# Performance work log

Hardware: AMD Instinct MI355X
Metric: run time of the kernel (lower is better)

## Reference

```python
import jax, jax.numpy as jnp
import numpy as np

DIM = 1024
NUM_HEADS = 16
HEAD_DIM = DIM // NUM_HEADS
SCALE = HEAD_DIM ** -0.5


def setup_inputs() -> dict:
    key = jax.random.key(0)
    ks = jax.random.split(key, 7)
    b, n = 2, 2048
    x = jax.random.normal(ks[0], (b, n, DIM), dtype=jnp.float32)
    s = DIM ** -0.5
    Wq = jax.random.normal(ks[1], (DIM, DIM), dtype=jnp.float32) * s
    bq = jax.random.normal(ks[2], (DIM,), dtype=jnp.float32) * 0.01
    Wk = jax.random.normal(ks[3], (DIM, DIM), dtype=jnp.float32) * s
    bk = jax.random.normal(ks[4], (DIM,), dtype=jnp.float32) * 0.01
    Wv = jax.random.normal(ks[5], (DIM, DIM), dtype=jnp.float32) * s
    bv = jax.random.normal(ks[6], (DIM,), dtype=jnp.float32) * 0.01
    return {"x": x, "Wq": Wq, "bq": bq, "Wk": Wk, "bk": bk, "Wv": Wv, "bv": bv}


def reference(x, Wq, bq, Wk, bk, Wv, bv):
    b, n, _ = x.shape
    # Linear projections (torch Linear: x @ W.T + b; here W stored as [in, out])
    q = x @ Wq + bq
    k = x @ Wk + bk
    v = x @ Wv + bv
    # split heads: [b, n, h*d] -> [b, h, n, d]
    split = lambda t: t.reshape(b, n, NUM_HEADS, HEAD_DIM).transpose(0, 2, 1, 3)
    q, k, v = split(q), split(k), split(v)
    sim = jnp.einsum('bhid,bhjd->bhij', q, k) * SCALE
    attn = jax.nn.softmax(sim, axis=-1)
    out = jnp.einsum('bhij,bhjd->bhid', attn, v)
    return out.transpose(0, 2, 1, 3).reshape(b, n, DIM)
```

## Files before the change

### kernel.cpp

```cpp
#include <hip/hip_runtime.h>
#include <cstdint>
#include <cstddef>

#define NB    2
#define SEQ   2048
#define DIMC  1024
#define NH    16
#define HDIM  64
#define MROWS (NB*SEQ)
#define NFEAT (3*DIMC)
#define KVBLK 64
#define NT    (SEQ/KVBLK)

typedef _Float16 half8 __attribute__((ext_vector_type(8)));
typedef _Float16 half4 __attribute__((ext_vector_type(4)));
typedef _Float16 half2v __attribute__((ext_vector_type(2)));
typedef __fp16   fp16x2 __attribute__((ext_vector_type(2)));
typedef float    f32x4 __attribute__((ext_vector_type(4)));

typedef const __attribute__((address_space(1))) void* gas_ptr;
typedef __attribute__((address_space(3))) void*       las_ptr;

__device__ __forceinline__ void gload_lds16(const void* g, void* l) {
    __builtin_amdgcn_global_load_lds((gas_ptr)g, (las_ptr)l, 16, 0, 0);
}

__device__ __forceinline__ int swz4(int r) { return (r ^ (r >> 2)) & 3; }

__device__ __forceinline__ float fast_exp2(float x) {
    float r;
    asm("v_exp_f32 %0, %1" : "=v"(r) : "v"(x));
    return r;
}

__device__ __forceinline__ half2v pk_f16(float a, float b) {
    fp16x2 r = __builtin_amdgcn_cvt_pkrtz(a, b);
    return __builtin_bit_cast(half2v, r);
}

__global__ __launch_bounds__(256) void k_convert_x(const float* __restrict__ x,
                                                   _Float16* __restrict__ x16) {
    int i = (blockIdx.x * 256 + threadIdx.x) * 4;
    float4 v = *reinterpret_cast<const float4*>(x + i);
    half4 h = { (_Float16)v.x, (_Float16)v.y, (_Float16)v.z, (_Float16)v.w };
    *reinterpret_cast<half4*>(x16 + i) = h;
}

__global__ __launch_bounds__(256) void k_transpose_w(const float* __restrict__ Wq,
                                                     const float* __restrict__ Wk,
                                                     const float* __restrict__ Wv,
                                                     _Float16* __restrict__ wt) {
    __shared__ float tile[64][65];
    const int bid  = blockIdx.x;
    const int midx = bid >> 8;
    const int t2   = bid & 255;
    const int i0   = (t2 >> 4) * 64;
    const int o0   = (t2 & 15) * 64;
    const float* W = (midx == 0) ? Wq : (midx == 1 ? Wk : Wv);
    const int tid  = threadIdx.x;
    #pragma unroll
    for (int p = 0; p < 4; ++p) {
        int id = p * 256 + tid;
        int r = id >> 4, c4 = (id & 15) * 4;
        float4 v = *reinterpret_cast<const float4*>(W + (size_t)(i0 + r) * DIMC + o0 + c4);
        tile[r][c4 + 0] = v.x; tile[r][c4 + 1] = v.y;
        tile[r][c4 + 2] = v.z; tile[r][c4 + 3] = v.w;
    }
    __syncthreads();
    #pragma unroll
    for (int p = 0; p < 4; ++p) {
        int id = p * 256 + tid;
        int oc = id >> 4, i4 = (id & 15) * 4;
        half4 h = { (_Float16)tile[i4 + 0][oc], (_Float16)tile[i4 + 1][oc],
                    (_Float16)tile[i4 + 2][oc], (_Float16)tile[i4 + 3][oc] };
        *reinterpret_cast<half4*>(wt + (size_t)(midx * DIMC + o0 + oc) * DIMC + i0 + i4) = h;
    }
}

__global__ __launch_bounds__(256) void k_qkv_gemm(
    const _Float16* __restrict__ x16, const _Float16* __restrict__ wt,
    const float* __restrict__ bq, const float* __restrict__ bk, const float* __restrict__ bv,
    _Float16* __restrict__ q16, _Float16* __restrict__ k16, _Float16* __restrict__ vt16)
{
    __shared__ __align__(16) char sraw[49152];
    const int tid = threadIdx.x;
    const int lane = tid & 63;
    const int w = tid >> 6, wm = w >> 1, wn = w & 1;
    const int lr = lane & 15, lg = lane >> 4;
    const int bn = blockIdx.x % (NFEAT / 128);
    const int bm = blockIdx.x / (NFEAT / 128);
    const int m0 = bm * 128, n0 = bn * 128;

    const f32x4 zero4 = {0.f, 0.f, 0.f, 0.f};
    f32x4 acc[4][4];
    #pragma unroll
    for (int i = 0; i < 4; ++i)
        #pragma unroll
        for (int j = 0; j < 4; ++j) acc[i][j] = zero4;

    auto stage = [&](int buf, int kt) {
        const int k0 = kt * 32;
        char* Adst = sraw + buf * 8192;
        char* Bdst = sraw + 24576 + buf * 8192;
        #pragma unroll
        for (int t = 0; t < 2; ++t) {
            int slot = t * 256 + tid;
            int row = slot >> 2, ch = slot & 3;
            int chg = ch ^ swz4(row);
            gload_lds16(x16 + (size_t)(m0 + row) * DIMC + k0 + chg * 8, Adst + slot * 16);
            gload_lds16(wt  + (size_t)(n0 + row) * DIMC + k0 + chg * 8, Bdst + slot * 16);
        }
    };

    stage(0, 0);
    stage(1, 1);
    for (int kt = 0; kt < DIMC / 32; ++kt) {
        if (kt < DIMC / 32 - 1) asm volatile("s_waitcnt vmcnt(4)" ::: "memory");
        else                    asm volatile("s_waitcnt vmcnt(0)" ::: "memory");
        __builtin_amdgcn_s_barrier();
        if (kt + 2 < DIMC / 32) stage((kt + 2) % 3, kt + 2);
        const char* Ab = sraw + (kt % 3) * 8192;
        const char* Bb = sraw + 24576 + (kt % 3) * 8192;
        half8 af[4], bf[4];
        #pragma unroll
        for (int mb = 0; mb < 4; ++mb) {
            int row = wm * 64 + mb * 16 + lr;
            af[mb] = *(const half8*)(Ab + row * 64 + ((lg ^ swz4(row)) << 4));
        }
        #pragma unroll
        for (int nb = 0; nb < 4; ++nb) {
            int col = wn * 64 + nb * 16 + lr;
            bf[nb] = *(const half8*)(Bb + col * 64 + ((lg ^ swz4(col)) << 4));
        }
        #pragma unroll
        for (int mb = 0; mb < 4; ++mb)
            #pragma unroll
            for (int nb = 0; nb < 4; ++nb)
                acc[mb][nb] = __builtin_amdgcn_mfma_f32_16x16x32_f16(af[mb], bf[nb], acc[mb][nb], 0, 0, 0);
    }

    const int sec = n0 >> 10;
    const float* bias = (sec == 0) ? bq : (sec == 1 ? bk : bv);
    const float scl = (sec == 0) ? 0.125f * 1.44269504088896f : 1.0f;
    float bfv[4];
    #pragma unroll
    for (int nb = 0; nb < 4; ++nb)
        bfv[nb] = bias[(n0 & 1023) + wn * 64 + nb * 16 + lr];

    if (sec < 2) {
        _Float16* dst = (sec == 0) ? q16 : k16;
        #pragma unroll
        for (int mb = 0; mb < 4; ++mb)
            #pragma unroll
            for (int i2 = 0; i2 < 4; ++i2) {
                int rg = m0 + wm * 64 + mb * 16 + lg * 4 + i2;
                int bb = rg >> 11, nn = rg & (SEQ - 1);
                #pragma unroll
                for (int nb = 0; nb < 4; ++nb) {
                    int f1 = (n0 & 1023) + wn * 64 + nb * 16 + lr;
                    int hh = f1 >> 6, dd = f1 & 63;
                    dst[((size_t)(bb * NH + hh) * SEQ + nn) * HDIM + dd] =
                        (_Float16)((acc[mb][nb][i2] + bfv[nb]) * scl);
                }
            }
    } else {
        __syncthreads();
        char* lt = sraw;
        #pragma unroll
        for (int mb = 0; mb < 4; ++mb)
            #pragma unroll
            for (int nb = 0; nb < 4; ++nb) {
                int c  = wn * 64 + nb * 16 + lr;
                int r0 = wm * 64 + mb * 16 + lg * 4;
                half4 hv = { (_Float16)(acc[mb][nb][0] + bfv[nb]),
                             (_Float16)(acc[mb][nb][1] + bfv[nb]),
                             (_Float16)(acc[mb][nb][2] + bfv[nb]),
                             (_Float16)(acc[mb][nb][3] + bfv[nb]) };
                *(half4*)(lt + c * 272 + r0 * 2) = hv;
            }
        __syncthreads();
        #pragma unroll
        for (int p = 0; p < 8; ++p) {
            int id = p * 256 + tid;
            int c = id >> 4, r8 = (id & 15) * 8;
            half8 hv = *(const half8*)(lt + c * 272 + r8 * 2);
            int f1 = (n0 & 1023) + c;
            int hh = f1 >> 6, dd = f1 & 63;
            int rg = m0 + r8;
            int bb = rg >> 11, nn = rg & (SEQ - 1);
            *(half8*)(vt16 + ((size_t)(bb * NH + hh) * HDIM + dd) * SEQ + nn) = hv;
        }
    }
}

__global__ __launch_bounds__(512, 4) void k_attn(
    const _Float16* __restrict__ q16, const _Float16* __restrict__ k16,
    const _Float16* __restrict__ vt16, float* __restrict__ out)
{
    __shared__ __align__(16) char lds[65536];
    const int tid = threadIdx.x, lane = tid & 63, w = tid >> 6;
    const int lr = lane & 15, lg = lane >> 4;
    const int sub = w >> 2;
    const int qg  = w & 3;
    const int swz = (blockIdx.x & 7) * 64 + (blockIdx.x >> 3);
    const int bh = swz >> 4;
    const int qt = swz & 15;
    const int qrow0 = qt * 128 + qg * 32;
    const _Float16* qh = q16 + (size_t)bh * SEQ * HDIM;
    const _Float16* kh = k16 + (size_t)bh * SEQ * HDIM;
    const _Float16* vh = vt16 + (size_t)bh * HDIM * SEQ;

    const int srow = tid >> 3;
    const int scg  = (tid & 7) ^ (srow & 7);

    auto stageKV = [&](int buf, int t) {
        const int jA = t * KVBLK, jB = (16 + t) * KVBLK;
        gload_lds16(kh + (size_t)(jA + srow) * HDIM + scg * 8,
                    lds + buf * 8192 + tid * 16);
        gload_lds16(kh + (size_t)(jB + srow) * HDIM + scg * 8,
                    lds + 16384 + buf * 8192 + tid * 16);
        gload_lds16(vh + (size_t)srow * SEQ + jA + scg * 8,
                    lds + 32768 + buf * 8192 + tid * 16);
        gload_lds16(vh + (size_t)srow * SEQ + jB + scg * 8,
                    lds + 49152 + buf * 8192 + tid * 16);
    };

    half8 aq[2][2];
    #pragma unroll
    for (int g = 0; g < 2; ++g)
        #pragma unroll
        for (int kc = 0; kc < 2; ++kc)
            aq[g][kc] = *(const half8*)(qh + (size_t)(qrow0 + g * 16 + lr) * HDIM + kc * 32 + lg * 8);

    const f32x4 zero4 = {0.f, 0.f, 0.f, 0.f};
    f32x4 l4[2] = { zero4, zero4 };
    f32x4 oacc[2][4];
    #pragma unroll
    for (int g = 0; g < 2; ++g)
        #pragma unroll
        for (int i = 0; i < 4; ++i) oacc[g][i] = zero4;

    stageKV(0, 0);
    for (int t = 0; t < 16; ++t) {
        __syncthreads();
        if (t + 1 < 16) stageKV((t + 1) & 1, t + 1);
        const char* Kb = lds + sub * 16384 + (t & 1) * 8192;
        const char* Vb = lds + 32768 + sub * 16384 + (t & 1) * 8192;

        f32x4 s0[4], s1[4];
        __builtin_amdgcn_s_setprio(1);
        #pragma unroll
        for (int jb = 0; jb < 4; ++jb) {
            int row = jb * 16 + lr;
            half8 k0 = *(const half8*)(Kb + row * 128 + (((0 + lg) ^ (row & 7)) << 4));
            half8 k1 = *(const half8*)(Kb + row * 128 + (((4 + lg) ^ (row & 7)) << 4));
            f32x4 a0 = __builtin_amdgcn_mfma_f32_16x16x32_f16(k0, aq[0][0], zero4, 0, 0, 0);
            f32x4 a1 = __builtin_amdgcn_mfma_f32_16x16x32_f16(k0, aq[1][0], zero4, 0, 0, 0);
            a0 = __builtin_amdgcn_mfma_f32_16x16x32_f16(k1, aq[0][1], a0, 0, 0, 0);
            a1 = __builtin_amdgcn_mfma_f32_16x16x32_f16(k1, aq[1][1], a1, 0, 0, 0);
            s0[jb] = a0; s1[jb] = a1;
        }
        __builtin_amdgcn_s_setprio(0);

        half4 pf0[4], pf1[4];
        #pragma unroll
        for (int jb = 0; jb < 4; ++jb) {
            #pragma unroll
            for (int i = 0; i < 4; ++i) s0[jb][i] = fast_exp2(s0[jb][i]);
            l4[0] += s0[jb];
            half2v w0 = pk_f16(s0[jb][0], s0[jb][1]);
            half2v w1 = pk_f16(s0[jb][2], s0[jb][3]);
            pf0[jb] = half4{ w0.x, w0.y, w1.x, w1.y };
        }
        #pragma unroll
        for (int jb = 0; jb < 4; ++jb) {
            #pragma unroll
            for (int i = 0; i < 4; ++i) s1[jb][i] = fast_exp2(s1[jb][i]);
            l4[1] += s1[jb];
            half2v w0 = pk_f16(s1[jb][0], s1[jb][1]);
            half2v w1 = pk_f16(s1[jb][2], s1[jb][3]);
            pf1[jb] = half4{ w0.x, w0.y, w1.x, w1.y };
        }

        __builtin_amdgcn_s_setprio(1);
        #pragma unroll
        for (int db = 0; db < 4; ++db) {
            int row = db * 16 + lr;
            const char* vrow = Vb + row * 128;
            #pragma unroll
            for (int jb = 0; jb < 4; ++jb) {
                half4 vf = *(const half4*)(vrow + (((jb * 2 + (lg >> 1)) ^ (row & 7)) << 4)
                                           + ((lg & 1) << 3));
                oacc[0][db] = __builtin_amdgcn_mfma_f32_16x16x16f16(pf0[jb], vf, oacc[0][db], 0, 0, 0);
                oacc[1][db] = __builtin_amdgcn_mfma_f32_16x16x16f16(pf1[jb], vf, oacc[1][db], 0, 0, 0);
            }
        }
        __builtin_amdgcn_s_setprio(0);
    }

    __syncthreads();
    char* xch = lds;
    if (sub == 1) {
        char* sl = xch + (qg * 2) * 5120;
        #pragma unroll
        for (int g = 0; g < 2; ++g) {
            #pragma unroll
            for (int db = 0; db < 4; ++db)
                *(f32x4*)(sl + g * 5120 + db * 1024 + lane * 16) = oacc[g][db];
            *(f32x4*)(sl + g * 5120 + 4096 + lane * 16) = l4[g];
        }
    }
    __syncthreads();
    if (sub == 0) {
        char* sl = xch + (qg * 2) * 5120;
        #pragma unroll
        for (int g = 0; g < 2; ++g) {
            #pragma unroll
            for (int db = 0; db < 4; ++db)
                oacc[g][db] += *(const f32x4*)(sl + g * 5120 + db * 1024 + lane * 16);
            l4[g] += *(const f32x4*)(sl + g * 5120 + 4096 + lane * 16);
        }
        const int bb = bh >> 4, hh = bh & 15;
        #pragma unroll
        for (int g = 0; g < 2; ++g) {
            float l_i = (l4[g][0] + l4[g][1]) + (l4[g][2] + l4[g][3]);
            l_i += __shfl_xor(l_i, 16);
            l_i += __shfl_xor(l_i, 32);
            float rlq[4];
            #pragma unroll
            for (int i = 0; i < 4; ++i)
                rlq[i] = 1.0f / __shfl(l_i, lg * 4 + i);
            #pragma unroll
            for (int db = 0; db < 4; ++db)
                #pragma unroll
                for (int i = 0; i < 4; ++i) {
                    int nn = qrow0 + g * 16 + lg * 4 + i;
                    out[((size_t)bb * SEQ + nn) * DIMC + hh * HDIM + db * 16 + lr] =
                        oacc[g][db][i] * rlq[i];
                }
        }
    }
}

extern "C" void kernel_launch(void* const* d_in, const int* in_sizes, int n_in,
                              void* d_out, int out_size, void* d_ws, size_t ws_size,
                              hipStream_t stream)
{
    const float* x  = (const float*)d_in[0];
    const float* Wq = (const float*)d_in[1];
    const float* bq = (const float*)d_in[2];
    const float* Wk = (const float*)d_in[3];
    const float* bk = (const float*)d_in[4];
    const float* Wv = (const float*)d_in[5];
    const float* bv = (const float*)d_in[6];
    float* out = (float*)d_out;

    char* ws = (char*)d_ws;
    _Float16* x16  = (_Float16*)ws;
    _Float16* wt   = (_Float16*)(ws + ((size_t)8  << 20));
    _Float16* q16  = (_Float16*)(ws + ((size_t)14 << 20));
    _Float16* k16  = (_Float16*)(ws + ((size_t)22 << 20));
    _Float16* vt16 = (_Float16*)(ws + ((size_t)30 << 20));

    k_convert_x<<<MROWS * DIMC / 1024, 256, 0, stream>>>(x, x16);
    k_transpose_w<<<3 * 256, 256, 0, stream>>>(Wq, Wk, Wv, wt);
    k_qkv_gemm<<<(MROWS / 128) * (NFEAT / 128), 256, 0, stream>>>(x16, wt, bq, bk, bv,
                                                                  q16, k16, vt16);
    k_attn<<<32 * (SEQ / 128), 512, 0, stream>>>(q16, k16, vt16, out);
}
```

Baseline: 94.55 us.

## Switch attention MFMAs to 32x32x16 tiles with cross-lane P repacking

Rewrites the attention kernel's QK^T and PV matmuls to use 32x32x16 f16 MFMA instructions instead of 16x16 shapes, so the score tile of 32 queries by 64 keys comes from fewer, larger instructions. Because the 32x32 accumulator layout does not match the A-operand layout needed for PV, the probabilities are packed to fp16 and rearranged across wave halves with xor-32 shuffles. The row-sum reduction, the cross-subgroup LDS exchange and the output store are changed to match the new layout. The aim is higher MFMA throughput and fewer LDS fragment loads, at the cost of extra shuffle and select instructions and a different register footprint.

```diff
diff --git a/kernel.cpp b/kernel.cpp
--- a/kernel.cpp
+++ b/kernel.cpp
@@ -10,13 +10,14 @@
 #define MROWS (NB*SEQ)
 #define NFEAT (3*DIMC)
 #define KVBLK 64
-#define NT    (SEQ/KVBLK)
 
 typedef _Float16 half8 __attribute__((ext_vector_type(8)));
 typedef _Float16 half4 __attribute__((ext_vector_type(4)));
 typedef _Float16 half2v __attribute__((ext_vector_type(2)));
 typedef __fp16   fp16x2 __attribute__((ext_vector_type(2)));
-typedef float    f32x4 __attribute__((ext_vector_type(4)));
+typedef float    f32x4  __attribute__((ext_vector_type(4)));
+typedef float    f32x16 __attribute__((ext_vector_type(16)));
+typedef uint32_t u32x4v __attribute__((ext_vector_type(4)));
 
 typedef const __attribute__((address_space(1))) void* gas_ptr;
 typedef __attribute__((address_space(3))) void*       las_ptr;
@@ -33,9 +34,9 @@
     return r;
 }
 
-__device__ __forceinline__ half2v pk_f16(float a, float b) {
+__device__ __forceinline__ uint32_t pk_u32(float a, float b) {
     fp16x2 r = __builtin_amdgcn_cvt_pkrtz(a, b);
-    return __builtin_bit_cast(half2v, r);
+    return __builtin_bit_cast(uint32_t, r);
 }
 
 __global__ __launch_bounds__(256) void k_convert_x(const float* __restrict__ x,
@@ -199,7 +200,7 @@
 {
     __shared__ __align__(16) char lds[65536];
     const int tid = threadIdx.x, lane = tid & 63, w = tid >> 6;
-    const int lr = lane & 15, lg = lane >> 4;
+    const int ln = lane & 31, h = lane >> 5;
     const int sub = w >> 2;
     const int qg  = w & 3;
     const int swz = (blockIdx.x & 7) * 64 + (blockIdx.x >> 3);
@@ -225,20 +226,15 @@
                     lds + 49152 + buf * 8192 + tid * 16);
     };
 
-    half8 aq[2][2];
-    #pragma unroll
-    for (int g = 0; g < 2; ++g)
-        #pragma unroll
-        for (int kc = 0; kc < 2; ++kc)
-            aq[g][kc] = *(const half8*)(qh + (size_t)(qrow0 + g * 16 + lr) * HDIM + kc * 32 + lg * 8);
-
-    const f32x4 zero4 = {0.f, 0.f, 0.f, 0.f};
-    f32x4 l4[2] = { zero4, zero4 };
-    f32x4 oacc[2][4];
-    #pragma unroll
-    for (int g = 0; g < 2; ++g)
-        #pragma unroll
-        for (int i = 0; i < 4; ++i) oacc[g][i] = zero4;
+    half8 aq[4];
+    #pragma unroll
+    for (int kdb = 0; kdb < 4; ++kdb)
+        aq[kdb] = *(const half8*)(qh + (size_t)(qrow0 + ln) * HDIM + kdb * 16 + h * 8);
+
+    f32x16 oacc[2];
+    #pragma unroll
+    for (int r = 0; r < 16; ++r) { oacc[0][r] = 0.f; oacc[1][r] = 0.f; }
+    float l_p = 0.f;
 
     stageKV(0, 0);
     for (int t = 0; t < 16; ++t) {
@@ -247,97 +243,104 @@
         const char* Kb = lds + sub * 16384 + (t & 1) * 8192;
         const char* Vb = lds + 32768 + sub * 16384 + (t & 1) * 8192;
 
-        f32x4 s0[4], s1[4];
+        f32x16 s[2];
+        #pragma unroll
+        for (int r = 0; r < 16; ++r) { s[0][r] = 0.f; s[1][r] = 0.f; }
         __builtin_amdgcn_s_setprio(1);
         #pragma unroll
-        for (int jb = 0; jb < 4; ++jb) {
-            int row = jb * 16 + lr;
-            half8 k0 = *(const half8*)(Kb + row * 128 + (((0 + lg) ^ (row & 7)) << 4));
-            half8 k1 = *(const half8*)(Kb + row * 128 + (((4 + lg) ^ (row & 7)) << 4));
-            f32x4 a0 = __builtin_amdgcn_mfma_f32_16x16x32_f16(k0, aq[0][0], zero4, 0, 0, 0);
-            f32x4 a1 = __builtin_amdgcn_mfma_f32_16x16x32_f16(k0, aq[1][0], zero4, 0, 0, 0);
-            a0 = __builtin_amdgcn_mfma_f32_16x16x32_f16(k1, aq[0][1], a0, 0, 0, 0);
-            a1 = __builtin_amdgcn_mfma_f32_16x16x32_f16(k1, aq[1][1], a1, 0, 0, 0);
-            s0[jb] = a0; s1[jb] = a1;
+        for (int kb = 0; kb < 2; ++kb) {
+            int row = kb * 32 + ln;
+            #pragma unroll
+            for (int kdb = 0; kdb < 4; ++kdb) {
+                half8 kf = *(const half8*)(Kb + row * 128 + (((kdb * 2 + h) ^ (ln & 7)) << 4));
+                s[kb] = __builtin_amdgcn_mfma_f32_32x32x16_f16(kf, aq[kdb], s[kb], 0, 0, 0);
+            }
         }
         __builtin_amdgcn_s_setprio(0);
 
-        half4 pf0[4], pf1[4];
-        #pragma unroll
-        for (int jb = 0; jb < 4; ++jb) {
-            #pragma unroll
-            for (int i = 0; i < 4; ++i) s0[jb][i] = fast_exp2(s0[jb][i]);
-            l4[0] += s0[jb];
-            half2v w0 = pk_f16(s0[jb][0], s0[jb][1]);
-            half2v w1 = pk_f16(s0[jb][2], s0[jb][3]);
-            pf0[jb] = half4{ w0.x, w0.y, w1.x, w1.y };
-        }
-        #pragma unroll
-        for (int jb = 0; jb < 4; ++jb) {
-            #pragma unroll
-            for (int i = 0; i < 4; ++i) s1[jb][i] = fast_exp2(s1[jb][i]);
-            l4[1] += s1[jb];
-            half2v w0 = pk_f16(s1[jb][0], s1[jb][1]);
-            half2v w1 = pk_f16(s1[jb][2], s1[jb][3]);
-            pf1[jb] = half4{ w0.x, w0.y, w1.x, w1.y };
+        #pragma unroll
+        for (int kb = 0; kb < 2; ++kb)
+            #pragma unroll
+            for (int r = 0; r < 16; ++r) {
+                s[kb][r] = fast_exp2(s[kb][r]);
+                l_p += s[kb][r];
+            }
+
+        uint32_t pa[16];
+        #pragma unroll
+        for (int kb = 0; kb < 2; ++kb) {
+            uint32_t c0 = pk_u32(s[kb][0],  s[kb][1]);
+            uint32_t c1 = pk_u32(s[kb][2],  s[kb][3]);
+            uint32_t c2 = pk_u32(s[kb][4],  s[kb][5]);
+            uint32_t c3 = pk_u32(s[kb][6],  s[kb][7]);
+            uint32_t c4 = pk_u32(s[kb][8],  s[kb][9]);
+            uint32_t c5 = pk_u32(s[kb][10], s[kb][11]);
+            uint32_t c6 = pk_u32(s[kb][12], s[kb][13]);
+            uint32_t c7 = pk_u32(s[kb][14], s[kb][15]);
+            uint32_t c0s = (uint32_t)__shfl_xor((int)c0, 32);
+            uint32_t c1s = (uint32_t)__shfl_xor((int)c1, 32);
+            uint32_t c2s = (uint32_t)__shfl_xor((int)c2, 32);
+            uint32_t c3s = (uint32_t)__shfl_xor((int)c3, 32);
+            uint32_t c4s = (uint32_t)__shfl_xor((int)c4, 32);
+            uint32_t c5s = (uint32_t)__shfl_xor((int)c5, 32);
+            uint32_t c6s = (uint32_t)__shfl_xor((int)c6, 32);
+            uint32_t c7s = (uint32_t)__shfl_xor((int)c7, 32);
+            pa[kb * 8 + 0] = h ? c2s : c0;
+            pa[kb * 8 + 1] = h ? c3s : c1;
+            pa[kb * 8 + 2] = h ? c2  : c0s;
+            pa[kb * 8 + 3] = h ? c3  : c1s;
+            pa[kb * 8 + 4] = h ? c6s : c4;
+            pa[kb * 8 + 5] = h ? c7s : c5;
+            pa[kb * 8 + 6] = h ? c6  : c4s;
+            pa[kb * 8 + 7] = h ? c7  : c5s;
         }
 
         __builtin_amdgcn_s_setprio(1);
         #pragma unroll
-        for (int db = 0; db < 4; ++db) {
-            int row = db * 16 + lr;
-            const char* vrow = Vb + row * 128;
-            #pragma unroll
-            for (int jb = 0; jb < 4; ++jb) {
-                half4 vf = *(const half4*)(vrow + (((jb * 2 + (lg >> 1)) ^ (row & 7)) << 4)
-                                           + ((lg & 1) << 3));
-                oacc[0][db] = __builtin_amdgcn_mfma_f32_16x16x16f16(pf0[jb], vf, oacc[0][db], 0, 0, 0);
-                oacc[1][db] = __builtin_amdgcn_mfma_f32_16x16x16f16(pf1[jb], vf, oacc[1][db], 0, 0, 0);
+        for (int db = 0; db < 2; ++db) {
+            int row = db * 32 + ln;
+            #pragma unroll
+            for (int kbp = 0; kbp < 4; ++kbp) {
+                half8 vf = *(const half8*)(Vb + row * 128 + (((kbp * 2 + h) ^ (ln & 7)) << 4));
+                u32x4v pu = { pa[kbp * 4 + 0], pa[kbp * 4 + 1], pa[kbp * 4 + 2], pa[kbp * 4 + 3] };
+                half8 pa8 = __builtin_bit_cast(half8, pu);
+                oacc[db] = __builtin_amdgcn_mfma_f32_32x32x16_f16(pa8, vf, oacc[db], 0, 0, 0);
             }
         }
         __builtin_amdgcn_s_setprio(0);
     }
 
     __syncthreads();
-    char* xch = lds;
+    float* xch = (float*)lds;
     if (sub == 1) {
-        char* sl = xch + (qg * 2) * 5120;
-        #pragma unroll
-        for (int g = 0; g < 2; ++g) {
-            #pragma unroll
-            for (int db = 0; db < 4; ++db)
-                *(f32x4*)(sl + g * 5120 + db * 1024 + lane * 16) = oacc[g][db];
-            *(f32x4*)(sl + g * 5120 + 4096 + lane * 16) = l4[g];
-        }
+        float* sl = xch + qg * 2112;
+        #pragma unroll
+        for (int db = 0; db < 2; ++db)
+            #pragma unroll
+            for (int r = 0; r < 16; ++r)
+                sl[(db * 16 + r) * 64 + lane] = oacc[db][r];
+        sl[32 * 64 + lane] = l_p;
     }
     __syncthreads();
     if (sub == 0) {
-        char* sl = xch + (qg * 2) * 5120;
-        #pragma unroll
-        for (int g = 0; g < 2; ++g) {
-            #pragma unroll
-            for (int db = 0; db < 4; ++db)
-                oacc[g][db] += *(const f32x4*)(sl + g * 5120 + db * 1024 + lane * 16);
-            l4[g] += *(const f32x4*)(sl + g * 5120 + 4096 + lane * 16);
-        }
+        float* sl = xch + qg * 2112;
+        #pragma unroll
+        for (int db = 0; db < 2; ++db)
+            #pragma unroll
+            for (int r = 0; r < 16; ++r)
+                oacc[db][r] += sl[(db * 16 + r) * 64 + lane];
+        l_p += sl[32 * 64 + lane];
+        l_p += __shfl_xor(l_p, 32);
+        float rl = 1.0f / l_p;
+
         const int bb = bh >> 4, hh = bh & 15;
         #pragma unroll
-        for (int g = 0; g < 2; ++g) {
-            float l_i = (l4[g][0] + l4[g][1]) + (l4[g][2] + l4[g][3]);
-            l_i += __shfl_xor(l_i, 16);
-            l_i += __shfl_xor(l_i, 32);
-            float rlq[4];
-            #pragma unroll
-            for (int i = 0; i < 4; ++i)
-                rlq[i] = 1.0f / __shfl(l_i, lg * 4 + i);
-            #pragma unroll
-            for (int db = 0; db < 4; ++db)
-                #pragma unroll
-                for (int i = 0; i < 4; ++i) {
-                    int nn = qrow0 + g * 16 + lg * 4 + i;
-                    out[((size_t)bb * SEQ + nn) * DIMC + hh * HDIM + db * 16 + lr] =
-                        oacc[g][db][i] * rlq[i];
-                }
+        for (int r = 0; r < 16; ++r) {
+            int qloc = (r & 3) + 8 * (r >> 2) + 4 * h;
+            float rlq = __shfl(rl, qloc);
+            int nn = qrow0 + qloc;
+            out[((size_t)bb * SEQ + nn) * DIMC + hh * HDIM + 0  + ln] = oacc[0][r] * rlq;
+            out[((size_t)bb * SEQ + nn) * DIMC + hh * HDIM + 32 + ln] = oacc[1][r] * rlq;
         }
     }
 }
```

Result: slower. 97.37 us (+3.0%).
